# Optimization experiments

Hardware: AMD Instinct MI355X
Metric: run time of the kernel (lower is better)

The kernel has to match this reference:

```python
import jax, jax.numpy as jnp
import numpy as np

def setup_inputs() -> dict:
    key = jax.random.key(0)
    kA, kB = jax.random.split(key)
    A = jax.random.normal(kA, (32, 4096, 256), dtype=jnp.float32)
    B = jax.random.normal(kB, (32, 4096, 256), dtype=jnp.float32)
    return {"A": A, "B": B}

def reference(A, B):
    # mean over s of outer products a_si (x) b_sj == (A^T @ B) / S
    S = A.shape[-2]
    return jnp.einsum('bsm,bsn->bmn', A, B) / S
```

## Files before the change

### kernel.cpp

```cpp
#include <hip/hip_runtime.h>


typedef __attribute__((ext_vector_type(8))) short  bf16x8;
typedef __attribute__((ext_vector_type(4))) float  f32x4;
typedef __attribute__((ext_vector_type(8))) ushort u16x8;
typedef __attribute__((ext_vector_type(4))) float  fvec4;

#define SEQ    4096
#define MD     256
#define KSPLIT 4
#define SCHUNK (SEQ / KSPLIT)
#define BK     64
#define NSTEP  (SCHUNK / BK)

#define FENCE() asm volatile("" ::: "memory")

__device__ __forceinline__ int swz(int m) { return ((m >> 2) ^ (m << 1)) & 15; }

__global__ __launch_bounds__(256, 2) void opm_kernel(const float* __restrict__ A,
                                                     const float* __restrict__ B,
                                                     float* __restrict__ out) {
    const int bid = blockIdx.x;
    const int grp = bid & 127;
    const int til = bid >> 7;
    const int b   = grp >> 2;
    const int kc  = grp & 3;
    const int mt  = til >> 1;
    const int nt  = til & 1;
    const int tid = threadIdx.x;

    __shared__ ushort ldsA[128 * 128];
    __shared__ ushort ldsB[128 * 128];

    const int c4 = tid & 31;
    const int sb = tid >> 5;
    const fvec4* gA = (const fvec4*)A + (size_t)b * (SEQ * MD / 4) + mt * 32 + c4;
    const fvec4* gB = (const fvec4*)B + (size_t)b * (SEQ * MD / 4) + nt * 32 + c4;
    const int s0 = kc * SCHUNK;

    const int lane = tid & 63;
    const int w    = tid >> 6;
    const int wm   = w >> 1, wn = w & 1;
    const int r16  = lane & 15, gq = lane >> 4;

    int mAr[4], nBr[4], f3a[4], f3b[4];
#pragma unroll
    for (int f = 0; f < 4; ++f) {
        mAr[f] = wm * 64 + f * 16 + r16;
        nBr[f] = wn * 64 + f * 16 + r16;
        f3a[f] = swz(mAr[f]);
        f3b[f] = swz(nBr[f]);
    }

    f32x4 acc[4][4] = {};
    fvec4 ra[2][4], rb[2][4];

    auto issue = [&](int st) {
        const int srow = s0 + st * BK;
#pragma unroll
        for (int it = 0; it < 2; ++it) {
            const int sl = (sb + 8 * it) * 4;
#pragma unroll
            for (int r = 0; r < 4; ++r) {
                ra[it][r] = gA[(size_t)(srow + sl + r) * (MD / 4)];
                rb[it][r] = gB[(size_t)(srow + sl + r) * (MD / 4)];
            }
        }
    };

    auto convert_write = [&]() {
#pragma unroll
        for (int it = 0; it < 2; ++it) {
            const int lg = sb + 8 * it;
#pragma unroll
            for (int j = 0; j < 4; ++j) {
                const int m = c4 * 4 + j;
                u16x8 va, vb;
#pragma unroll
                for (int r = 0; r < 4; ++r) {
                    const float xa = ra[it][r][j];
                    const uint  ua = __float_as_uint(xa);
                    const float la = xa - __uint_as_float(ua & 0xffff0000u);
                    va[r]     = (ushort)(ua >> 16);
                    va[4 + r] = (ushort)(__float_as_uint(la) >> 16);
                    const float xb = rb[it][r][j];
                    const uint  ub = __float_as_uint(xb);
                    const float lb = xb - __uint_as_float(ub & 0xffff0000u);
                    vb[r]     = (ushort)(ub >> 16);
                    vb[4 + r] = (ushort)(__float_as_uint(lb) >> 16);
                }
                const int idx = m * 128 + ((lg ^ swz(m)) * 8);
                *(u16x8*)&ldsA[idx] = va;
                *(u16x8*)&ldsB[idx] = vb;
            }
        }
    };

    issue(0);

    for (int st = 0; st < NSTEP; ++st) {
        convert_write();
        if (st + 1 < NSTEP) issue(st + 1);
        FENCE();
        asm volatile("s_waitcnt lgkmcnt(0)" ::: "memory");
        __builtin_amdgcn_s_barrier();
        FENCE();

#pragma unroll
        for (int q = 0; q < 4; ++q) {
            bf16x8 bq[4];
#pragma unroll
            for (int fn = 0; fn < 4; ++fn) {
                const int pg = (q * 4 + gq) ^ f3b[fn];
                bq[fn] = *(const bf16x8*)&ldsB[nBr[fn] * 128 + pg * 8];
            }
#pragma unroll
            for (int fm = 0; fm < 4; ++fm) {
                const int pg = (q * 4 + gq) ^ f3a[fm];
                bf16x8 a   = *(const bf16x8*)&ldsA[mAr[fm] * 128 + pg * 8];
                bf16x8 asw = __builtin_shufflevector(a, a, 4, 5, 6, 7, 0, 1, 2, 3);
#pragma unroll
                for (int fn = 0; fn < 4; ++fn) {
                    acc[fm][fn] = __builtin_amdgcn_mfma_f32_16x16x32_bf16(
                        a, bq[fn], acc[fm][fn], 0, 0, 0);
                    acc[fm][fn] = __builtin_amdgcn_mfma_f32_16x16x32_bf16(
                        asw, bq[fn], acc[fm][fn], 0, 0, 0);
                }
            }
        }

        FENCE();
        __builtin_amdgcn_s_barrier();
        FENCE();
    }

    const float inv = 1.0f / (float)SEQ;
    float* ob = out + (size_t)b * (MD * MD) + (size_t)(mt * 128) * MD + nt * 128;
#pragma unroll
    for (int fm = 0; fm < 4; ++fm) {
#pragma unroll
        for (int fn = 0; fn < 4; ++fn) {
#pragma unroll
            for (int r = 0; r < 4; ++r) {
                const int row = wm * 64 + fm * 16 + gq * 4 + r;
                const int col = wn * 64 + fn * 16 + r16;
                unsafeAtomicAdd(&ob[row * MD + col], acc[fm][fn][r] * inv);
            }
        }
    }
}

extern "C" void kernel_launch(void* const* d_in, const int* in_sizes, int n_in,
                              void* d_out, int out_size, void* d_ws, size_t ws_size,
                              hipStream_t stream) {
    const float* A = (const float*)d_in[0];
    const float* B = (const float*)d_in[1];
    float* out     = (float*)d_out;

    hipMemsetAsync(d_out, 0, (size_t)out_size * sizeof(float), stream);

    dim3 grid(512);
    dim3 block(256);
    hipLaunchKernelGGL(opm_kernel, grid, block, 0, stream, A, B, out);
}
```

Baseline: 298.4 us.

## Use 512-thread blocks with 32x32x16 MFMA tiles and per-thread single load group

Block size goes from 256 to 512 threads with 8 waves in a 2x4 layout. Each wave now computes 64x32 using 32x32x16 bf16 MFMAs instead of 64x64 with 16x16x32, and each thread loads one 4-row group per step instead of two. This lowers per-thread register pressure and raises the number of waves in flight to hide global-load latency. LDS use per block is unchanged, so occupancy now depends on whether two 64KB blocks fit per CU, and the (512,4) launch bound may force register limits.

```diff
diff --git a/kernel.cpp b/kernel.cpp
--- a/kernel.cpp
+++ b/kernel.cpp
@@ -1,10 +1,10 @@
 #include <hip/hip_runtime.h>
 
 
-typedef __attribute__((ext_vector_type(8))) short  bf16x8;
-typedef __attribute__((ext_vector_type(4))) float  f32x4;
-typedef __attribute__((ext_vector_type(8))) ushort u16x8;
-typedef __attribute__((ext_vector_type(4))) float  fvec4;
+typedef __attribute__((ext_vector_type(8)))  short  bf16x8;
+typedef __attribute__((ext_vector_type(16))) float  f32x16;
+typedef __attribute__((ext_vector_type(8)))  ushort u16x8;
+typedef __attribute__((ext_vector_type(4)))  float  fvec4;
 
 #define SEQ    4096
 #define MD     256
@@ -17,16 +17,14 @@
 
 __device__ __forceinline__ int swz(int m) { return ((m >> 2) ^ (m << 1)) & 15; }
 
-__global__ __launch_bounds__(256, 2) void opm_kernel(const float* __restrict__ A,
+__global__ __launch_bounds__(512, 4) void opm_kernel(const float* __restrict__ A,
                                                      const float* __restrict__ B,
                                                      float* __restrict__ out) {
     const int bid = blockIdx.x;
     const int grp = bid & 127;
     const int til = bid >> 7;
-    const int b   = grp >> 2;
-    const int kc  = grp & 3;
-    const int mt  = til >> 1;
-    const int nt  = til & 1;
+    const int b  = grp >> 2, kc = grp & 3;
+    const int mt = til >> 1, nt = til & 1;
     const int tid = threadIdx.x;
 
     __shared__ ushort ldsA[128 * 128];
@@ -39,94 +37,72 @@
     const int s0 = kc * SCHUNK;
 
     const int lane = tid & 63;
-    const int w    = tid >> 6;
-    const int wm   = w >> 1, wn = w & 1;
-    const int r16  = lane & 15, gq = lane >> 4;
+    const int w   = tid >> 6;
+    const int wm  = w >> 2, wn = w & 3;
+    const int l31 = lane & 31, lh = lane >> 5;
 
-    int mAr[4], nBr[4], f3a[4], f3b[4];
-#pragma unroll
-    for (int f = 0; f < 4; ++f) {
-        mAr[f] = wm * 64 + f * 16 + r16;
-        nBr[f] = wn * 64 + f * 16 + r16;
-        f3a[f] = swz(mAr[f]);
-        f3b[f] = swz(nBr[f]);
-    }
+    const int rowA0 = wm * 64 + l31;
+    const int rowA1 = rowA0 + 32;
+    const int rowB  = wn * 32 + l31;
+    const int sA0 = swz(rowA0), sA1 = swz(rowA1), sB = swz(rowB);
 
-    f32x4 acc[4][4] = {};
-    fvec4 ra[2][4], rb[2][4];
+    f32x16 acc0 = {}, acc1 = {};
+    fvec4 ra[4], rb[4];
 
     auto issue = [&](int st) {
-        const int srow = s0 + st * BK;
+        const int srow = s0 + st * BK + sb * 4;
 #pragma unroll
-        for (int it = 0; it < 2; ++it) {
-            const int sl = (sb + 8 * it) * 4;
-#pragma unroll
-            for (int r = 0; r < 4; ++r) {
-                ra[it][r] = gA[(size_t)(srow + sl + r) * (MD / 4)];
-                rb[it][r] = gB[(size_t)(srow + sl + r) * (MD / 4)];
-            }
-        }
-    };
-
-    auto convert_write = [&]() {
-#pragma unroll
-        for (int it = 0; it < 2; ++it) {
-            const int lg = sb + 8 * it;
-#pragma unroll
-            for (int j = 0; j < 4; ++j) {
-                const int m = c4 * 4 + j;
-                u16x8 va, vb;
-#pragma unroll
-                for (int r = 0; r < 4; ++r) {
-                    const float xa = ra[it][r][j];
-                    const uint  ua = __float_as_uint(xa);
-                    const float la = xa - __uint_as_float(ua & 0xffff0000u);
-                    va[r]     = (ushort)(ua >> 16);
-                    va[4 + r] = (ushort)(__float_as_uint(la) >> 16);
-                    const float xb = rb[it][r][j];
-                    const uint  ub = __float_as_uint(xb);
-                    const float lb = xb - __uint_as_float(ub & 0xffff0000u);
-                    vb[r]     = (ushort)(ub >> 16);
-                    vb[4 + r] = (ushort)(__float_as_uint(lb) >> 16);
-                }
-                const int idx = m * 128 + ((lg ^ swz(m)) * 8);
-                *(u16x8*)&ldsA[idx] = va;
-                *(u16x8*)&ldsB[idx] = vb;
-            }
+        for (int r = 0; r < 4; ++r) {
+            ra[r] = gA[(size_t)(srow + r) * (MD / 4)];
+            rb[r] = gB[(size_t)(srow + r) * (MD / 4)];
         }
     };
 
     issue(0);
 
     for (int st = 0; st < NSTEP; ++st) {
-        convert_write();
+        u16x8 va[4], vb[4];
+#pragma unroll
+        for (int j = 0; j < 4; ++j) {
+#pragma unroll
+            for (int r = 0; r < 4; ++r) {
+                const float xa = ra[r][j];
+                const uint  ua = __float_as_uint(xa);
+                const float la = xa - __uint_as_float(ua & 0xffff0000u);
+                va[j][r]     = (ushort)(ua >> 16);
+                va[j][4 + r] = (ushort)(__float_as_uint(la) >> 16);
+                const float xb = rb[r][j];
+                const uint  ub = __float_as_uint(xb);
+                const float lb = xb - __uint_as_float(ub & 0xffff0000u);
+                vb[j][r]     = (ushort)(ub >> 16);
+                vb[j][4 + r] = (ushort)(__float_as_uint(lb) >> 16);
+            }
+        }
         if (st + 1 < NSTEP) issue(st + 1);
+#pragma unroll
+        for (int j = 0; j < 4; ++j) {
+            const int m   = c4 * 4 + j;
+            const int idx = m * 128 + ((sb ^ swz(m)) * 8);
+            *(u16x8*)&ldsA[idx] = va[j];
+            *(u16x8*)&ldsB[idx] = vb[j];
+        }
         FENCE();
         asm volatile("s_waitcnt lgkmcnt(0)" ::: "memory");
         __builtin_amdgcn_s_barrier();
         FENCE();
 
 #pragma unroll
-        for (int q = 0; q < 4; ++q) {
-            bf16x8 bq[4];
-#pragma unroll
-            for (int fn = 0; fn < 4; ++fn) {
-                const int pg = (q * 4 + gq) ^ f3b[fn];
-                bq[fn] = *(const bf16x8*)&ldsB[nBr[fn] * 128 + pg * 8];
-            }
-#pragma unroll
-            for (int fm = 0; fm < 4; ++fm) {
-                const int pg = (q * 4 + gq) ^ f3a[fm];
-                bf16x8 a   = *(const bf16x8*)&ldsA[mAr[fm] * 128 + pg * 8];
-                bf16x8 asw = __builtin_shufflevector(a, a, 4, 5, 6, 7, 0, 1, 2, 3);
-#pragma unroll
-                for (int fn = 0; fn < 4; ++fn) {
-                    acc[fm][fn] = __builtin_amdgcn_mfma_f32_16x16x32_bf16(
-                        a, bq[fn], acc[fm][fn], 0, 0, 0);
-                    acc[fm][fn] = __builtin_amdgcn_mfma_f32_16x16x32_bf16(
-                        asw, bq[fn], acc[fm][fn], 0, 0, 0);
-                }
-            }
+        for (int kk = 0; kk < 8; ++kk) {
+            const int g = kk * 2 + lh;
+            bf16x8 bf = *(const bf16x8*)&ldsB[rowB  * 128 + ((g ^ sB)  * 8)];
+            bf16x8 a0 = *(const bf16x8*)&ldsA[rowA0 * 128 + ((g ^ sA0) * 8)];
+            bf16x8 a1 = *(const bf16x8*)&ldsA[rowA1 * 128 + ((g ^ sA1) * 8)];
+            acc0 = __builtin_amdgcn_mfma_f32_32x32x16_bf16(a0, bf, acc0, 0, 0, 0);
+            acc1 = __builtin_amdgcn_mfma_f32_32x32x16_bf16(a1, bf, acc1, 0, 0, 0);
+            const bf16x8 w0 = __builtin_shufflevector(a0, a0, 4, 5, 6, 7, 0, 1, 2, 3);
+            const bf16x8 w1 = __builtin_shufflevector(a1, a1, 4, 5, 6, 7, 0, 1, 2, 3);
+            acc0 = __builtin_amdgcn_mfma_f32_32x32x16_bf16(w0, bf, acc0, 0, 0, 0);
+            acc1 = __builtin_amdgcn_mfma_f32_32x32x16_bf16(w1, bf, acc1, 0, 0, 0);
         }
 
         FENCE();
@@ -135,17 +111,16 @@
     }
 
     const float inv = 1.0f / (float)SEQ;
-    float* ob = out + (size_t)b * (MD * MD) + (size_t)(mt * 128) * MD + nt * 128;
+    const int   colb = nt * 128 + wn * 32 + l31;
+    float* ob = out + (size_t)b * (MD * MD);
 #pragma unroll
-    for (int fm = 0; fm < 4; ++fm) {
+    for (int tm = 0; tm < 2; ++tm) {
+        const int rbase = mt * 128 + wm * 64 + tm * 32 + 4 * lh;
+        const f32x16 av = tm ? acc1 : acc0;
 #pragma unroll
-        for (int fn = 0; fn < 4; ++fn) {
-#pragma unroll
-            for (int r = 0; r < 4; ++r) {
-                const int row = wm * 64 + fm * 16 + gq * 4 + r;
-                const int col = wn * 64 + fn * 16 + r16;
-                unsafeAtomicAdd(&ob[row * MD + col], acc[fm][fn][r] * inv);
-            }
+        for (int reg = 0; reg < 16; ++reg) {
+            const int row = rbase + (reg & 3) + 8 * (reg >> 2);
+            unsafeAtomicAdd(&ob[row * MD + colb], av[reg] * inv);
         }
     }
 }
@@ -160,6 +135,6 @@
     hipMemsetAsync(d_out, 0, (size_t)out_size * sizeof(float), stream);
 
     dim3 grid(512);
-    dim3 block(256);
+    dim3 block(512);
     hipLaunchKernelGGL(opm_kernel, grid, block, 0, stream, A, B, out);
 }
```

After: 327.7 us. 1.1x slower.
